# Optimization experiments

Measured on AMD Instinct MI355X. Metric: run time of the kernel, lower is better.

Reference implementation:

```python
import jax, jax.numpy as jnp
import numpy as np

B, N, C = 2, 4096, 512
NUM_HEADS = 8
HEAD_DIM = C // NUM_HEADS
SCALE = HEAD_DIM ** -0.5
THETA = 10000.0


def setup_inputs() -> dict:
    key = jax.random.key(0)
    ks = jax.random.split(key, 5)
    x = jax.random.normal(ks[0], (B, N, C), dtype=jnp.float32)
    Wqkv = jax.random.normal(ks[1], (3 * C, C), dtype=jnp.float32) * 0.02
    bqkv = jax.random.normal(ks[2], (3 * C,), dtype=jnp.float32) * 0.02
    Wproj = jax.random.normal(ks[3], (C, C), dtype=jnp.float32) * 0.02
    bproj = jax.random.normal(ks[4], (C,), dtype=jnp.float32) * 0.02
    return {"x": x, "Wqkv": Wqkv, "bqkv": bqkv, "Wproj": Wproj, "bproj": bproj}


def _rope(x, seq_len, head_dim):
    # x: [B, H, N, head_dim]; interleaved rotary embedding
    freqs = 1.0 / THETA ** (jnp.arange(0, head_dim, 2, dtype=jnp.float32) / head_dim)  # [hd/2]
    t = jnp.arange(seq_len, dtype=jnp.float32)
    freqs_cis = jnp.outer(t, freqs)                      # [N, hd/2]
    sin_f = jnp.sin(freqs_cis)
    cos_f = jnp.cos(freqs_cis)
    x_even = x[..., ::2]                                 # [B, H, N, hd/2]
    x_odd = x[..., 1::2]
    rot = jnp.stack(
        [x_even * cos_f - x_odd * sin_f,
         x_even * sin_f + x_odd * cos_f],
        axis=-1,
    )                                                    # [B, H, N, hd/2, 2]
    return rot.reshape(x.shape)


def reference(x, Wqkv, bqkv, Wproj, bproj):
    b, n, c = x.shape
    # fused QKV projection: y = x @ W.T + b
    qkv = x @ Wqkv.T + bqkv                              # [B, N, 3C]
    qkv = qkv.reshape(b, n, 3, NUM_HEADS, HEAD_DIM)
    qkv = jnp.transpose(qkv, (2, 0, 3, 1, 4))            # [3, B, H, N, hd]
    q, k, v = qkv[0], qkv[1], qkv[2]
    q = _rope(q, n, HEAD_DIM)
    k = _rope(k, n, HEAD_DIM)
    attn = jnp.einsum('bhqd,bhkd->bhqk', q, k) * SCALE   # [B, H, N, N]
    attn = jax.nn.softmax(attn, axis=-1)
    out = jnp.einsum('bhqk,bhkd->bhqd', attn, v)         # [B, H, N, hd]
    out = jnp.transpose(out, (0, 2, 1, 3)).reshape(b, n, c)
    return out @ Wproj.T + bproj
```

## Files before the change

kernel.cpp:

```cpp
#include <hip/hip_runtime.h>
#include <hip/hip_bf16.h>
#include <stdint.h>

#define B_ 2
#define N_ 4096
#define C_ 512
#define H_ 8
#define D_ 64
#define M_ (B_*N_)
#define K3_ (3*C_)
#define NCH 4

typedef __attribute__((ext_vector_type(8)))  short short8;
typedef __attribute__((ext_vector_type(4)))  float f32x4;
typedef __attribute__((ext_vector_type(16))) float f32x16;

static __device__ __forceinline__ unsigned short f2bf(float f) {
  union { float f; unsigned u; } cv; cv.f = f;
  unsigned r = cv.u + 0x7fffu + ((cv.u >> 16) & 1u);
  return (unsigned short)(r >> 16);
}
static __device__ __forceinline__ float bf2f(short x) {
  union { unsigned u; float f; } cv;
  cv.u = ((unsigned)(unsigned short)x) << 16;
  return cv.f;
}
static __device__ __forceinline__ float fexp2(float x) {
#if __has_builtin(__builtin_amdgcn_exp2f)
  return __builtin_amdgcn_exp2f(x);
#else
  return exp2f(x);
#endif
}
static __device__ __forceinline__ unsigned cvt_pk_bf16(float a, float b) {
  unsigned r;
  asm("v_cvt_pk_bf16_f32 %0, %1, %2" : "=v"(r) : "v"(a), "v"(b));
  return r;
}
static __device__ __forceinline__ void gload_lds16(const void* g, void* l) {
  __builtin_amdgcn_global_load_lds((const __attribute__((address_space(1))) unsigned*)g,
                                   (__attribute__((address_space(3))) unsigned*)l, 16, 0, 0);
}
static __device__ __forceinline__ f32x16 zero16() {
  f32x16 z;
#pragma unroll
  for (int i = 0; i < 16; i++) z[i] = 0.f;
  return z;
}

__global__ void prep(const float* __restrict__ x, const float* __restrict__ Wqkv,
                     const float* __restrict__ Wproj,
                     short* __restrict__ xb, short* __restrict__ wqkvb,
                     short* __restrict__ wprjb, float2* __restrict__ tab) {
  int blk = blockIdx.x, t = threadIdx.x;
  if (blk < 4096) {
    int i = blk * 256 + t;
    float4 v = ((const float4*)x)[i];
    short4 o;
    o.x = (short)f2bf(v.x); o.y = (short)f2bf(v.y);
    o.z = (short)f2bf(v.z); o.w = (short)f2bf(v.w);
    ((short4*)xb)[i] = o;
  } else if (blk < 4864) {
    int i = (blk - 4096) * 256 + t;
    float4 v = ((const float4*)Wqkv)[i];
    short4 o;
    o.x = (short)f2bf(v.x); o.y = (short)f2bf(v.y);
    o.z = (short)f2bf(v.z); o.w = (short)f2bf(v.w);
    ((short4*)wqkvb)[i] = o;
  } else if (blk < 5120) {
    int i = (blk - 4864) * 256 + t;
    float4 v = ((const float4*)Wproj)[i];
    short4 o;
    o.x = (short)f2bf(v.x); o.y = (short)f2bf(v.y);
    o.z = (short)f2bf(v.z); o.w = (short)f2bf(v.w);
    ((short4*)wprjb)[i] = o;
  } else {
    int i = (blk - 5120) * 256 + t;
    int p = i & 31, n = i >> 5;
    float freq = exp2f(-((float)(2 * p) / 64.0f) * 13.287712379549449f);
    float ang = (float)n * freq;
    float s, c;
    sincosf(ang, &s, &c);
    float2 r; r.x = c; r.y = s;
    tab[i] = r;
  }
}

__global__ void rope_vt(const short* __restrict__ qkvb, const float2* __restrict__ tab,
                        short* __restrict__ Qf, short* __restrict__ Kf,
                        short* __restrict__ Vf) {
  __shared__ short tile[128][72];
  int blk = blockIdx.x, t = threadIdx.x;
  if (blk < 1024) {
    int tk = blk >> 9;
    int bh = (blk & 511) >> 5;
    int nb4 = blk & 31;
    int b = bh >> 3, h = bh & 7;
    int n0 = nb4 * 128;
#pragma unroll
    for (int pass = 0; pass < 4; pass++) {
      int row = pass * 32 + (t >> 3), chunk = t & 7;
      short8 v = *(const short8*)(qkvb + (size_t)(b * N_ + n0 + row) * K3_ + tk * C_ + h * D_ + chunk * 8);
      *(short8*)&tile[row][chunk * 8] = v;
    }
    __syncthreads();
    int lane = t & 63, f = t >> 6;
    int c = lane & 31, hi = lane >> 5;
    int d0 = f * 16 + hi * 8;
    float sc = (tk == 0) ? 0.18033688011112042f : 1.0f;
    short* base = (tk ? Kf : Qf);
#pragma unroll
    for (int i = 0; i < 4; i++) {
      int n_l = i * 32 + c;
      short8 v = *(const short8*)&tile[n_l][d0];
      const float2* tp = tab + (size_t)(n0 + n_l) * 32 + (d0 >> 1);
      short8 w;
#pragma unroll
      for (int j = 0; j < 4; j++) {
        float e = bf2f(v[2 * j]), o = bf2f(v[2 * j + 1]);
        float2 cs = tp[j];
        float e2 = (e * cs.x - o * cs.y) * sc;
        float o2 = (e * cs.y + o * cs.x) * sc;
        w[2 * j] = (short)f2bf(e2);
        w[2 * j + 1] = (short)f2bf(o2);
      }
      short* dst = base + (((size_t)(bh * 128 + nb4 * 4 + i) * 4 + f) * 512) + lane * 8;
      *(short8*)dst = w;
    }
  } else {
    int blk2 = blk - 1024;
    int bh = blk2 >> 7, kblk = blk2 & 127;
    int b = bh >> 3, h = bh & 7;
    int n0 = kblk * 32;
    {
      int row = t >> 3, c8 = t & 7;
      short8 v = *(const short8*)(qkvb + (size_t)(b * N_ + n0 + row) * K3_ + 2 * C_ + h * D_ + c8 * 8);
      *(short8*)&tile[row][c8 * 8] = v;
    }
    __syncthreads();
    {
      int frag = t >> 6, lane = t & 63;
      int hi = lane >> 5, c = lane & 31;
      int g = frag & 1, dblk = frag >> 1;
      short8 w;
#pragma unroll
      for (int j = 0; j < 8; j++) w[j] = tile[g * 16 + hi * 8 + j][dblk * 32 + c];
      *(short8*)(Vf + ((size_t)(bh * 128 + kblk) * 4 + frag) * 512 + lane * 8) = w;
    }
  }
}

template<int OUTF32, int MFR>
__global__ __launch_bounds__(256) void gemm_bt(const short* __restrict__ A, const short* __restrict__ Bw,
                                               const float* __restrict__ bias, void* __restrict__ Cout,
                                               int M, int Nout, int K) {
  __shared__ short As[MFR * 32 * 64];
  __shared__ short Bs[128 * 64];
  int t = threadIdx.x, lane = t & 63, w = t >> 6, wr = w >> 1, wc = w & 1;
  int tM = blockIdx.x * (MFR * 32), tN = blockIdx.y * 128;
  int lrow = lane & 15, lhi = lane >> 4;
  int rs = (lrow & 7) * 8;
  f32x4 acc[MFR][4];
#pragma unroll
  for (int fm = 0; fm < MFR; fm++)
#pragma unroll
    for (int fn = 0; fn < 4; fn++)
#pragma unroll
      for (int r = 0; r < 4; r++) acc[fm][fn][r] = 0.f;

  int srow = t >> 3;
  int sq = ((t & 7) * 8) ^ ((srow & 7) * 8);

  for (int k0 = 0; k0 < K; k0 += 64) {
#pragma unroll
    for (int p = 0; p < MFR; p++)
      gload_lds16(A + (size_t)(tM + p * 32 + srow) * K + k0 + sq, As + p * 2048 + t * 8);
#pragma unroll
    for (int p = 0; p < 4; p++)
      gload_lds16(Bw + (size_t)(tN + p * 32 + srow) * K + k0 + sq, Bs + p * 2048 + t * 8);
    __syncthreads();
#pragma unroll
    for (int kk = 0; kk < 2; kk++) {
      int ko = (kk * 32 + lhi * 8) ^ rs;
      short8 af[MFR], bfr[4];
#pragma unroll
      for (int f = 0; f < MFR; f++)
        af[f] = *(const short8*)(As + (wr * (MFR * 16) + f * 16 + lrow) * 64 + ko);
#pragma unroll
      for (int f = 0; f < 4; f++)
        bfr[f] = *(const short8*)(Bs + (wc * 64 + f * 16 + lrow) * 64 + ko);
#pragma unroll
      for (int fm = 0; fm < MFR; fm++)
#pragma unroll
        for (int fn = 0; fn < 4; fn++)
          acc[fm][fn] = __builtin_amdgcn_mfma_f32_16x16x32_bf16(af[fm], bfr[fn], acc[fm][fn], 0, 0, 0);
    }
    __syncthreads();
  }

#pragma unroll
  for (int fn = 0; fn < 4; fn++) {
    int col = tN + wc * 64 + fn * 16 + lrow;
    float bv = bias[col];
#pragma unroll
    for (int fm = 0; fm < MFR; fm++) {
      int row0 = tM + wr * (MFR * 16) + fm * 16 + lhi * 4;
#pragma unroll
      for (int r = 0; r < 4; r++) {
        float v = acc[fm][fn][r] + bv;
        if (OUTF32) ((float*)Cout)[(size_t)(row0 + r) * Nout + col] = v;
        else        ((short*)Cout)[(size_t)(row0 + r) * Nout + col] = (short)f2bf(v);
      }
    }
  }
}

static __device__ __forceinline__ f32x16 qk4(const short8* k, const short8* q, const f32x16& z0) {
  __builtin_amdgcn_s_setprio(1);
  f32x16 st = __builtin_amdgcn_mfma_f32_32x32x16_bf16(k[0], q[0], z0, 0, 0, 0);
  st = __builtin_amdgcn_mfma_f32_32x32x16_bf16(k[1], q[1], st, 0, 0, 0);
  st = __builtin_amdgcn_mfma_f32_32x32x16_bf16(k[2], q[2], st, 0, 0, 0);
  st = __builtin_amdgcn_mfma_f32_32x32x16_bf16(k[3], q[3], st, 0, 0, 0);
  __builtin_amdgcn_s_setprio(0);
  return st;
}
static __device__ __forceinline__ void soft_pv(const f32x16& st, const short8* v,
                                               f32x16& o0, f32x16& o1, float& lsum) {
  float ls = 0.f;
  unsigned cpk[8];
#pragma unroll
  for (int q2 = 0; q2 < 4; q2++) {
    float e0 = fexp2(st[4 * q2]),     e1 = fexp2(st[4 * q2 + 1]);
    float e2 = fexp2(st[4 * q2 + 2]), e3 = fexp2(st[4 * q2 + 3]);
    ls += (e0 + e1) + (e2 + e3);
    cpk[2 * q2]     = cvt_pk_bf16(e0, e1);
    cpk[2 * q2 + 1] = cvt_pk_bf16(e2, e3);
  }
  lsum += ls;
  unsigned w00 = cpk[0], w02 = cpk[2];
  asm volatile("v_permlane32_swap_b32 %0, %1" : "+v"(w00), "+v"(w02));
  unsigned w01 = cpk[1], w03 = cpk[3];
  asm volatile("v_permlane32_swap_b32 %0, %1" : "+v"(w01), "+v"(w03));
  unsigned w10 = cpk[4], w12 = cpk[6];
  asm volatile("v_permlane32_swap_b32 %0, %1" : "+v"(w10), "+v"(w12));
  unsigned w11 = cpk[5], w13 = cpk[7];
  asm volatile("v_permlane32_swap_b32 %0, %1" : "+v"(w11), "+v"(w13));
  union { unsigned u[4]; short8 s; } u0, u1;
  u0.u[0] = w00; u0.u[1] = w01; u0.u[2] = w02; u0.u[3] = w03;
  u1.u[0] = w10; u1.u[1] = w11; u1.u[2] = w12; u1.u[3] = w13;
  __builtin_amdgcn_s_setprio(1);
  o0 = __builtin_amdgcn_mfma_f32_32x32x16_bf16(u0.s, v[0], o0, 0, 0, 0);
  o0 = __builtin_amdgcn_mfma_f32_32x32x16_bf16(u1.s, v[1], o0, 0, 0, 0);
  o1 = __builtin_amdgcn_mfma_f32_32x32x16_bf16(u0.s, v[2], o1, 0, 0, 0);
  o1 = __builtin_amdgcn_mfma_f32_32x32x16_bf16(u1.s, v[3], o1, 0, 0, 0);
  __builtin_amdgcn_s_setprio(0);
}

__global__ __launch_bounds__(256, 2) void attn(const short* __restrict__ Qf, const short* __restrict__ Kf,
                                               const short* __restrict__ Vf,
                                               short* __restrict__ Op, float* __restrict__ lp) {
  __shared__ short Ks[2][4096];
  __shared__ short Vs[2][4096];
  int bh = blockIdx.x;
  int ch = blockIdx.z;
  int t = threadIdx.x;
  int wv = t >> 6, lane = t & 63;
  int c = lane & 31, hi = lane >> 5;
  int q0 = blockIdx.y * 256 + wv * 64;
  const int nkb2 = N_ / (NCH * 64);
  int kb0 = ch * (N_ / (NCH * 32));

  const short* QbA = Qf + ((size_t)(bh * 128 + (q0 >> 5)) * 4) * 512 + lane * 8;
  const short* Kg = Kf + ((size_t)(bh * 128 + kb0) * 4) * 512 + t * 8;
  const short* Vg = Vf + ((size_t)(bh * 128 + kb0) * 4) * 512 + t * 8;

  short8 qA[4], qB[4];
#pragma unroll
  for (int f = 0; f < 4; f++) qA[f] = *(const short8*)(QbA + f * 512);
#pragma unroll
  for (int f = 0; f < 4; f++) qB[f] = *(const short8*)(QbA + (4 + f) * 512);

  const f32x16 z0 = zero16();
  f32x16 oA0 = z0, oA1 = z0;
  f32x16 oB0 = z0, oB1 = z0;
  float lsA = 0.f, lsB = 0.f;

  gload_lds16(Kg,        &Ks[0][t * 8]);
  gload_lds16(Kg + 2048, &Ks[0][2048 + t * 8]);
  gload_lds16(Vg,        &Vs[0][t * 8]);
  gload_lds16(Vg + 2048, &Vs[0][2048 + t * 8]);
  __syncthreads();

  int buf = 0;
  for (int it = 0; it < nkb2; ++it) {
    if (it + 1 < nkb2) {
      const short* Kn = Kg + (size_t)(it + 1) * 4096;
      const short* Vn = Vg + (size_t)(it + 1) * 4096;
      gload_lds16(Kn,        &Ks[buf ^ 1][t * 8]);
      gload_lds16(Kn + 2048, &Ks[buf ^ 1][2048 + t * 8]);
      gload_lds16(Vn,        &Vs[buf ^ 1][t * 8]);
      gload_lds16(Vn + 2048, &Vs[buf ^ 1][2048 + t * 8]);
    }
#pragma unroll
    for (int s = 0; s < 2; s++) {
      short8 kf[4], vf[4];
#pragma unroll
      for (int f = 0; f < 4; f++) kf[f] = *(const short8*)&Ks[buf][s * 2048 + f * 512 + lane * 8];
#pragma unroll
      for (int f = 0; f < 4; f++) vf[f] = *(const short8*)&Vs[buf][s * 2048 + f * 512 + lane * 8];
      f32x16 stA = qk4(kf, qA, z0);
      f32x16 stB = qk4(kf, qB, z0);
      soft_pv(stA, vf, oA0, oA1, lsA);
      soft_pv(stB, vf, oB0, oB1, lsB);
    }
    __syncthreads();
    buf ^= 1;
  }

  float ltA = lsA + __shfl_xor(lsA, 32);
  float ltB = lsB + __shfl_xor(lsB, 32);
  float* lrow = lp + ((size_t)ch * 16 + bh) * N_ + q0;
  short* obase = Op + ((size_t)ch * 16 + bh) * N_ * D_;
  if (hi == 0) {
    lrow[c] = ltA;
    lrow[32 + c] = ltB;
  }
#pragma unroll
  for (int r = 0; r < 16; r++) {
    int ql = (r & 3) + 8 * (r >> 2) + 4 * hi;
    size_t nA = (size_t)(q0 + ql) * D_;
    size_t nB = (size_t)(q0 + 32 + ql) * D_;
    obase[nA + c]      = (short)f2bf(oA0[r]);
    obase[nA + 32 + c] = (short)f2bf(oA1[r]);
    obase[nB + c]      = (short)f2bf(oB0[r]);
    obase[nB + 32 + c] = (short)f2bf(oB1[r]);
  }
}

__global__ void combine(const short* __restrict__ Op, const float* __restrict__ lp,
                        short* __restrict__ AO) {
  int i = blockIdx.x * blockDim.x + threadIdx.x;
  if (i >= 16 * N_ * 8) return;
  int d8 = i & 7, q = (i >> 3) & (N_ - 1), bh = i >> 15;
  const size_t chs = (size_t)16 * N_ * D_;
  size_t base = ((size_t)bh * N_ + q) * D_ + d8 * 8;
  float acc[8];
#pragma unroll
  for (int j = 0; j < 8; j++) acc[j] = 0.f;
  float l = 0.f;
#pragma unroll
  for (int chv = 0; chv < NCH; chv++) {
    short8 v = *(const short8*)(Op + chv * chs + base);
#pragma unroll
    for (int j = 0; j < 8; j++) acc[j] += bf2f(v[j]);
    l += lp[((size_t)chv * 16 + bh) * N_ + q];
  }
  float inv = 1.0f / l;
  int bb = bh >> 3, h = bh & 7;
  short8 o;
#pragma unroll
  for (int j = 0; j < 8; j++) o[j] = (short)f2bf(acc[j] * inv);
  *(short8*)(AO + ((size_t)(bb * N_ + q)) * C_ + h * D_ + d8 * 8) = o;
}

extern "C" void kernel_launch(void* const* d_in, const int* in_sizes, int n_in,
                              void* d_out, int out_size, void* d_ws, size_t ws_size,
                              hipStream_t stream) {
  const float* x     = (const float*)d_in[0];
  const float* Wqkv  = (const float*)d_in[1];
  const float* bqkv  = (const float*)d_in[2];
  const float* Wproj = (const float*)d_in[3];
  const float* bproj = (const float*)d_in[4];
  float* out = (float*)d_out;
  char* ws = (char*)d_ws;

  const size_t off_wprjb = 0;
  const size_t off_tab   = 524288;
  const size_t off_q     = 1572864;
  const size_t off_k     = 9961472;
  const size_t off_vt    = 18350080;
  const size_t off_ao    = 26738688;
  const size_t off_xb    = 35127296;
  const size_t off_wqkvb = 43515904;
  const size_t off_qkvb  = 45088768;
  const size_t off_op    = 35127296;
  const size_t off_l     = 68681728;
  if (ws_size < 70254592) return;

  short* xb    = (short*)(ws + off_xb);
  short* wqkvb = (short*)(ws + off_wqkvb);
  short* wprjb = (short*)(ws + off_wprjb);
  short* qkvb  = (short*)(ws + off_qkvb);
  short* Qfp   = (short*)(ws + off_q);
  short* Kfp   = (short*)(ws + off_k);
  short* Vfp   = (short*)(ws + off_vt);
  short* AOp   = (short*)(ws + off_ao);
  float2* tab  = (float2*)(ws + off_tab);
  short* Opp   = (short*)(ws + off_op);
  float* lpp   = (float*)(ws + off_l);

  prep<<<dim3(5632), dim3(256), 0, stream>>>(x, Wqkv, Wproj, xb, wqkvb, wprjb, tab);

  gemm_bt<0, 4><<<dim3(64, 12), dim3(256), 0, stream>>>(xb, wqkvb, bqkv, qkvb, M_, K3_, C_);

  rope_vt<<<dim3(3072), dim3(256), 0, stream>>>(qkvb, tab, Qfp, Kfp, Vfp);

  attn<<<dim3(16, 16, NCH), dim3(256), 0, stream>>>(Qfp, Kfp, Vfp, Opp, lpp);
  combine<<<dim3(2048), dim3(256), 0, stream>>>(Opp, lpp, AOp);

  gemm_bt<1, 2><<<dim3(128, 4), dim3(256), 0, stream>>>(AOp, wprjb, bproj, (void*)out, M_, C_, C_);
}
```

Before: 136.5 us.

## Fuse split-KV combine into projection GEMM and halve attention key chunks

```diff
diff --git a/kernel.cpp b/kernel.cpp
--- a/kernel.cpp
+++ b/kernel.cpp
@@ -9,7 +9,7 @@
 #define D_ 64
 #define M_ (B_*N_)
 #define K3_ (3*C_)
-#define NCH 4
+#define NCH 2
 
 typedef __attribute__((ext_vector_type(8)))  short short8;
 typedef __attribute__((ext_vector_type(4)))  float f32x4;
@@ -150,19 +150,18 @@
   }
 }
 
-template<int OUTF32, int MFR>
-__global__ __launch_bounds__(256) void gemm_bt(const short* __restrict__ A, const short* __restrict__ Bw,
-                                               const float* __restrict__ bias, void* __restrict__ Cout,
-                                               int M, int Nout, int K) {
-  __shared__ short As[MFR * 32 * 64];
+__global__ __launch_bounds__(256) void gemm_qkv(const short* __restrict__ A, const short* __restrict__ Bw,
+                                                const float* __restrict__ bias, short* __restrict__ Cout,
+                                                int M, int Nout, int K) {
+  __shared__ short As[4 * 32 * 64];
   __shared__ short Bs[128 * 64];
   int t = threadIdx.x, lane = t & 63, w = t >> 6, wr = w >> 1, wc = w & 1;
-  int tM = blockIdx.x * (MFR * 32), tN = blockIdx.y * 128;
+  int tM = blockIdx.x * 128, tN = blockIdx.y * 128;
   int lrow = lane & 15, lhi = lane >> 4;
   int rs = (lrow & 7) * 8;
-  f32x4 acc[MFR][4];
-#pragma unroll
-  for (int fm = 0; fm < MFR; fm++)
+  f32x4 acc[4][4];
+#pragma unroll
+  for (int fm = 0; fm < 4; fm++)
 #pragma unroll
     for (int fn = 0; fn < 4; fn++)
 #pragma unroll
@@ -173,7 +172,7 @@
 
   for (int k0 = 0; k0 < K; k0 += 64) {
 #pragma unroll
-    for (int p = 0; p < MFR; p++)
+    for (int p = 0; p < 4; p++)
       gload_lds16(A + (size_t)(tM + p * 32 + srow) * K + k0 + sq, As + p * 2048 + t * 8);
 #pragma unroll
     for (int p = 0; p < 4; p++)
@@ -182,15 +181,15 @@
 #pragma unroll
     for (int kk = 0; kk < 2; kk++) {
       int ko = (kk * 32 + lhi * 8) ^ rs;
-      short8 af[MFR], bfr[4];
-#pragma unroll
-      for (int f = 0; f < MFR; f++)
-        af[f] = *(const short8*)(As + (wr * (MFR * 16) + f * 16 + lrow) * 64 + ko);
+      short8 af[4], bfr[4];
+#pragma unroll
+      for (int f = 0; f < 4; f++)
+        af[f] = *(const short8*)(As + (wr * 64 + f * 16 + lrow) * 64 + ko);
 #pragma unroll
       for (int f = 0; f < 4; f++)
         bfr[f] = *(const short8*)(Bs + (wc * 64 + f * 16 + lrow) * 64 + ko);
 #pragma unroll
-      for (int fm = 0; fm < MFR; fm++)
+      for (int fm = 0; fm < 4; fm++)
 #pragma unroll
         for (int fn = 0; fn < 4; fn++)
           acc[fm][fn] = __builtin_amdgcn_mfma_f32_16x16x32_bf16(af[fm], bfr[fn], acc[fm][fn], 0, 0, 0);
@@ -203,14 +202,88 @@
     int col = tN + wc * 64 + fn * 16 + lrow;
     float bv = bias[col];
 #pragma unroll
-    for (int fm = 0; fm < MFR; fm++) {
-      int row0 = tM + wr * (MFR * 16) + fm * 16 + lhi * 4;
+    for (int fm = 0; fm < 4; fm++) {
+      int row0 = tM + wr * 64 + fm * 16 + lhi * 4;
 #pragma unroll
       for (int r = 0; r < 4; r++) {
         float v = acc[fm][fn][r] + bv;
-        if (OUTF32) ((float*)Cout)[(size_t)(row0 + r) * Nout + col] = v;
-        else        ((short*)Cout)[(size_t)(row0 + r) * Nout + col] = (short)f2bf(v);
+        Cout[(size_t)(row0 + r) * Nout + col] = (short)f2bf(v);
       }
+    }
+  }
+}
+
+__global__ __launch_bounds__(256) void gemm_proj(const short* __restrict__ Op, const float* __restrict__ lp,
+                                                 const short* __restrict__ Bw, const float* __restrict__ bias,
+                                                 float* __restrict__ Cout) {
+  __shared__ short As[2 * 32 * 64];
+  __shared__ short Bs[128 * 64];
+  const size_t chs = (size_t)16 * N_ * D_;
+  int t = threadIdx.x, lane = t & 63, w = t >> 6, wr = w >> 1, wc = w & 1;
+  int tM = blockIdx.x * 64, tN = blockIdx.y * 128;
+  int lrow = lane & 15, lhi = lane >> 4;
+  int rs = (lrow & 7) * 8;
+  f32x4 acc[2][4];
+#pragma unroll
+  for (int fm = 0; fm < 2; fm++)
+#pragma unroll
+    for (int fn = 0; fn < 4; fn++)
+#pragma unroll
+      for (int r = 0; r < 4; r++) acc[fm][fn][r] = 0.f;
+
+  int srow = t >> 3;
+  int sq = ((t & 7) * 8) ^ ((srow & 7) * 8);
+
+  for (int k0 = 0; k0 < C_; k0 += 64) {
+    int h = k0 >> 6;
+#pragma unroll
+    for (int p = 0; p < 2; p++) {
+      int m = tM + p * 32 + srow;
+      int b = m >> 12, q = m & (N_ - 1);
+      size_t lidx = (size_t)(b * H_ + h) * N_ + q;
+      float l = lp[lidx] + lp[(size_t)16 * N_ + lidx];
+      float inv = 1.0f / l;
+      size_t obase = ((size_t)(b * H_ + h) * N_ + q) * D_ + sq;
+      short8 v0 = *(const short8*)(Op + obase);
+      short8 v1 = *(const short8*)(Op + chs + obase);
+      short8 wv;
+#pragma unroll
+      for (int j = 0; j < 8; j++) wv[j] = (short)f2bf((bf2f(v0[j]) + bf2f(v1[j])) * inv);
+      *(short8*)(As + p * 2048 + t * 8) = wv;
+    }
+#pragma unroll
+    for (int p = 0; p < 4; p++)
+      gload_lds16(Bw + (size_t)(tN + p * 32 + srow) * C_ + k0 + sq, Bs + p * 2048 + t * 8);
+    __syncthreads();
+#pragma unroll
+    for (int kk = 0; kk < 2; kk++) {
+      int ko = (kk * 32 + lhi * 8) ^ rs;
+      short8 af[2], bfr[4];
+#pragma unroll
+      for (int f = 0; f < 2; f++)
+        af[f] = *(const short8*)(As + (wr * 32 + f * 16 + lrow) * 64 + ko);
+#pragma unroll
+      for (int f = 0; f < 4; f++)
+        bfr[f] = *(const short8*)(Bs + (wc * 64 + f * 16 + lrow) * 64 + ko);
+#pragma unroll
+      for (int fm = 0; fm < 2; fm++)
+#pragma unroll
+        for (int fn = 0; fn < 4; fn++)
+          acc[fm][fn] = __builtin_amdgcn_mfma_f32_16x16x32_bf16(af[fm], bfr[fn], acc[fm][fn], 0, 0, 0);
+    }
+    __syncthreads();
+  }
+
+#pragma unroll
+  for (int fn = 0; fn < 4; fn++) {
+    int col = tN + wc * 64 + fn * 16 + lrow;
+    float bv = bias[col];
+#pragma unroll
+    for (int fm = 0; fm < 2; fm++) {
+      int row0 = tM + wr * 32 + fm * 16 + lhi * 4;
+#pragma unroll
+      for (int r = 0; r < 4; r++)
+        Cout[(size_t)(row0 + r) * C_ + col] = acc[fm][fn][r] + bv;
     }
   }
 }
@@ -337,32 +410,6 @@
   }
 }
 
-__global__ void combine(const short* __restrict__ Op, const float* __restrict__ lp,
-                        short* __restrict__ AO) {
-  int i = blockIdx.x * blockDim.x + threadIdx.x;
-  if (i >= 16 * N_ * 8) return;
-  int d8 = i & 7, q = (i >> 3) & (N_ - 1), bh = i >> 15;
-  const size_t chs = (size_t)16 * N_ * D_;
-  size_t base = ((size_t)bh * N_ + q) * D_ + d8 * 8;
-  float acc[8];
-#pragma unroll
-  for (int j = 0; j < 8; j++) acc[j] = 0.f;
-  float l = 0.f;
-#pragma unroll
-  for (int chv = 0; chv < NCH; chv++) {
-    short8 v = *(const short8*)(Op + chv * chs + base);
-#pragma unroll
-    for (int j = 0; j < 8; j++) acc[j] += bf2f(v[j]);
-    l += lp[((size_t)chv * 16 + bh) * N_ + q];
-  }
-  float inv = 1.0f / l;
-  int bb = bh >> 3, h = bh & 7;
-  short8 o;
-#pragma unroll
-  for (int j = 0; j < 8; j++) o[j] = (short)f2bf(acc[j] * inv);
-  *(short8*)(AO + ((size_t)(bb * N_ + q)) * C_ + h * D_ + d8 * 8) = o;
-}
-
 extern "C" void kernel_launch(void* const* d_in, const int* in_sizes, int n_in,
                               void* d_out, int out_size, void* d_ws, size_t ws_size,
                               hipStream_t stream) {
@@ -379,7 +426,6 @@
   const size_t off_q     = 1572864;
   const size_t off_k     = 9961472;
   const size_t off_vt    = 18350080;
-  const size_t off_ao    = 26738688;
   const size_t off_xb    = 35127296;
   const size_t off_wqkvb = 43515904;
   const size_t off_qkvb  = 45088768;
@@ -394,19 +440,17 @@
   short* Qfp   = (short*)(ws + off_q);
   short* Kfp   = (short*)(ws + off_k);
   short* Vfp   = (short*)(ws + off_vt);
-  short* AOp   = (short*)(ws + off_ao);
   float2* tab  = (float2*)(ws + off_tab);
   short* Opp   = (short*)(ws + off_op);
   float* lpp   = (float*)(ws + off_l);
 
   prep<<<dim3(5632), dim3(256), 0, stream>>>(x, Wqkv, Wproj, xb, wqkvb, wprjb, tab);
 
-  gemm_bt<0, 4><<<dim3(64, 12), dim3(256), 0, stream>>>(xb, wqkvb, bqkv, qkvb, M_, K3_, C_);
+  gemm_qkv<<<dim3(64, 12), dim3(256), 0, stream>>>(xb, wqkvb, bqkv, qkvb, M_, K3_, C_);
 
   rope_vt<<<dim3(3072), dim3(256), 0, stream>>>(qkvb, tab, Qfp, Kfp, Vfp);
 
   attn<<<dim3(16, 16, NCH), dim3(256), 0, stream>>>(Qfp, Kfp, Vfp, Opp, lpp);
-  combine<<<dim3(2048), dim3(256), 0, stream>>>(Opp, lpp, AOp);
-
-  gemm_bt<1, 2><<<dim3(128, 4), dim3(256), 0, stream>>>(AOp, wprjb, bproj, (void*)out, M_, C_, C_);
-}
+
+  gemm_proj<<<dim3(128, 4), dim3(256), 0, stream>>>(Opp, lpp, wprjb, bproj, out);
+}
```

After: 135.9 us. Within noise of the previous version (-0.4%).
